# Performance work log

Measured on AMD Instinct MI355X. Metric: run time of the kernel, lower is better.

Reference implementation:

```python
import jax, jax.numpy as jnp
import numpy as np

B, S, E, H = 2, 2048, 1024, 16
D = E // H


def setup_inputs() -> dict:
    key = jax.random.key(0)
    ks = jax.random.split(key, 11)
    def lin(k):
        kw, kb = jax.random.split(k)
        bound = 1.0 / np.sqrt(E)
        W = jax.random.uniform(kw, (E, E), jnp.float32, -bound, bound)
        b = jax.random.uniform(kb, (E,), jnp.float32, -bound, bound)
        return W, b
    Wq, bq = lin(ks[0])
    Wk, bk = lin(ks[1])
    Wv, bv = lin(ks[2])
    Wo, bo = lin(ks[3])
    return {
        "query": jax.random.normal(ks[4], (B, S, E), jnp.float32),
        "key": jax.random.normal(ks[5], (B, S, E), jnp.float32),
        "value": jax.random.normal(ks[6], (B, S, E), jnp.float32),
        "Wq": Wq, "bq": bq, "Wk": Wk, "bk": bk,
        "Wv": Wv, "bv": bv, "Wo": Wo, "bo": bo,
        "is_causal": 1,
    }


def reference(query, key, value, Wq, bq, Wk, bk, Wv, bv, Wo, bo, is_causal):
    scale = D ** -0.5
    def heads(x, W, b):
        # torch Linear: x @ W.T + b, then [B,S,H,D] -> [B,H,S,D]
        y = jnp.einsum('bse,fe->bsf', x, W) + b
        return y.reshape(B, S, H, D).transpose(0, 2, 1, 3)
    q = heads(query, Wq, bq)
    k = heads(key, Wk, bk)
    v = heads(value, Wv, bv)
    scores = jnp.einsum('bhqd,bhkd->bhqk', q, k) * scale  # [B,H,S,S]
    if is_causal:
        mask = jnp.tril(jnp.ones((S, S), dtype=bool))
        scores = jnp.where(mask, scores, -jnp.inf)
    attn = jax.nn.softmax(scores, axis=-1)
    out = jnp.einsum('bhqk,bhkd->bhqd', attn, v)
    out = out.transpose(0, 2, 1, 3).reshape(B, S, E)
    return jnp.einsum('bse,fe->bsf', out, Wo) + bo
```

## Files before the change

kernel.cpp:

```cpp
#include <hip/hip_runtime.h>
#include <cstdint>
#include <cstddef>

typedef unsigned short u16;
typedef unsigned int u32;
typedef __attribute__((ext_vector_type(8))) short bf16x8;
typedef __attribute__((ext_vector_type(4))) float f32x4;
typedef __attribute__((ext_vector_type(16))) float f32x16;
typedef __attribute__((ext_vector_type(4))) u16 u16x4;
typedef __attribute__((ext_vector_type(4))) u32 u32x4;
typedef __attribute__((ext_vector_type(2))) u32 u32x2;

__device__ __forceinline__ u16 f2bf(float f) {
  u32 x = __builtin_bit_cast(u32, f);
  x += 0x7fffu + ((x >> 16) & 1u);
  return (u16)(x >> 16);
}

__device__ __forceinline__ void g2lds16(const u16* g, u16* l) {
  __builtin_amdgcn_global_load_lds(
      (const __attribute__((address_space(1))) u32*)g,
      (__attribute__((address_space(3))) u32*)l, 16, 0, 0);
}

struct CvtArgs { const float* s[7]; u16* d[7]; int n4[7]; };

__global__ __launch_bounds__(256) void cvt_all(CvtArgs a) {
  int y = blockIdx.y;
  const float4* __restrict__ src = (const float4*)a.s[y];
  u16* __restrict__ dst = a.d[y];
  int n4 = a.n4[y];
  for (int i = blockIdx.x * blockDim.x + threadIdx.x; i < n4;
       i += gridDim.x * blockDim.x) {
    float4 v = src[i];
    u16x4 o = { f2bf(v.x), f2bf(v.y), f2bf(v.z), f2bf(v.w) };
    *(u16x4*)(dst + (size_t)i * 4) = o;
  }
}

struct GemmArgs {
  const u16* A[3]; const u16* W[3]; const float* bias[3];
  void* out[3]; float scale[3]; int mode[3];
};

__global__ __launch_bounds__(256) void gemm_fused(GemmArgs ga) {
  __shared__ alignas(16) u16 As[2][128 * 32];
  __shared__ alignas(16) u16 Bs[2][128 * 32];
  const int z = blockIdx.z;
  const u16* __restrict__ A = ga.A[z];
  const u16* __restrict__ W = ga.W[z];
  const int tid = threadIdx.x;
  const int lane = tid & 63;
  const int w = tid >> 6;
  const int lo4 = lane & 15, hi2 = lane >> 4;
  const int l = (int)blockIdx.x + 8 * (int)blockIdx.y;
  const int wl = (l & 7) * 32 + (l >> 3);
  const int m0 = (wl >> 3) * 128;
  const int n0 = (wl & 7) * 128;
  const int wr = w >> 1, wc = w & 1;

  f32x4 acc[4][4] = {};

  auto stage = [&](int kt, int buf) {
    const int k0 = kt * 32;
#pragma unroll
    for (int i = 0; i < 2; ++i) {
      int c = (i * 4 + w) * 64 + lane;
      int r = c >> 2;
      int q = (c & 3) ^ ((r >> 1) & 3);
      g2lds16(A + (size_t)(m0 + r) * 1024 + k0 + q * 8, As[buf] + (i * 4 + w) * 512);
      g2lds16(W + (size_t)(n0 + r) * 1024 + k0 + q * 8, Bs[buf] + (i * 4 + w) * 512);
    }
  };

  stage(0, 0);
  stage(1, 1);
  for (int kt = 0; kt < 32; ++kt) {
    const int cur = kt & 1;
    asm volatile("s_waitcnt vmcnt(4)" ::: "memory");
    __builtin_amdgcn_s_barrier();
    bf16x8 af[4], bfr[4];
#pragma unroll
    for (int i = 0; i < 4; ++i) {
      int r = wr * 64 + i * 16 + lo4;
      int q = hi2 ^ ((r >> 1) & 3);
      af[i] = *(const bf16x8*)(As[cur] + r * 32 + q * 8);
    }
#pragma unroll
    for (int j = 0; j < 4; ++j) {
      int r = wc * 64 + j * 16 + lo4;
      int q = hi2 ^ ((r >> 1) & 3);
      bfr[j] = *(const bf16x8*)(Bs[cur] + r * 32 + q * 8);
    }
#pragma unroll
    for (int i = 0; i < 4; ++i)
#pragma unroll
      for (int j = 0; j < 4; ++j)
        acc[i][j] = __builtin_amdgcn_mfma_f32_16x16x32_bf16(af[i], bfr[j], acc[i][j], 0, 0, 0);
    __builtin_amdgcn_s_barrier();
    stage(kt + 2 < 32 ? kt + 2 : kt, cur);
  }
  asm volatile("s_waitcnt vmcnt(0)" ::: "memory");

  const float* __restrict__ bias = ga.bias[z];
  const float cs = ga.scale[z];
  const int mode = ga.mode[z];
#pragma unroll
  for (int j = 0; j < 4; ++j) {
    int n = n0 + wc * 64 + j * 16 + lo4;
    float bv = bias[n];
#pragma unroll
    for (int i = 0; i < 4; ++i) {
#pragma unroll
      for (int rg = 0; rg < 4; ++rg) {
        int m = m0 + wr * 64 + i * 16 + hi2 * 4 + rg;
        float v = (acc[i][j][rg] + bv) * cs;
        if (mode == 2) {
          ((float*)ga.out[z])[(size_t)m * 1024 + n] = v;
        } else {
          int b = m >> 11, s = m & 2047, h = n >> 6, d = n & 63;
          size_t addr = (mode == 0)
            ? ((size_t)(b * 16 + h) * 2048 + s) * 64 + d
            : ((size_t)(b * 16 + h) * 64 + d) * 2048 + s;
          ((u16*)ga.out[z])[addr] = f2bf(v);
        }
      }
    }
  }
}

__global__ __launch_bounds__(256, 2) void attn_kernel(
    const u16* __restrict__ Q, const u16* __restrict__ K,
    const u16* __restrict__ Vt, u16* __restrict__ Out,
    const int* __restrict__ causal_p) {
  __shared__ alignas(16) u16 Ks[2][2][64 * 64];
  __shared__ alignas(16) u16 Vs[2][2][64 * 64];
  const int tid = threadIdx.x, lane = tid & 63, w = tid >> 6;
  const int wg = w >> 1, wv = w & 1;
  const int ql = lane & 31, hi = lane >> 5;
  const int L = (int)blockIdx.x + 16 * (int)blockIdx.y;
  const int j = L >> 3;
  const int bh = (L & 7) * 4 + (j >> 4);
  const int slot = j & 15;
  const int qt = (j < 32) ? slot : 15 - slot;
  const int causal = *causal_p;
  const u16* Qb = Q + (size_t)bh * 2048 * 64;
  const u16* Kb = K + (size_t)bh * 2048 * 64;
  const u16* Vb = Vt + (size_t)bh * 64 * 2048;

  const int qA = qt * 128 + wv * 64 + ql;
  const int qB = qA + 32;

  bf16x8 qfA[4], qfB[4];
#pragma unroll
  for (int dsl = 0; dsl < 4; ++dsl) {
    qfA[dsl] = *(const bf16x8*)(Qb + (size_t)qA * 64 + dsl * 16 + hi * 8);
    qfB[dsl] = *(const bf16x8*)(Qb + (size_t)qB * 64 + dsl * 16 + hi * 8);
  }

  auto stageKV = [&](int jt, int buf) {
#pragma unroll
    for (int i = 0; i < 4; ++i) {
      int c = i * 128 + wv * 64 + lane;
      int r = c >> 3;
      int q = (c & 7) ^ (r & 7);
      g2lds16(Kb + (size_t)(jt * 64 + r) * 64 + q * 8, Ks[wg][buf] + (i * 128 + wv * 64) * 8);
      g2lds16(Vb + (size_t)r * 2048 + jt * 64 + q * 8, Vs[wg][buf] + (i * 128 + wv * 64) * 8);
    }
  };

  const int nt_w = causal ? (2 * qt + wv + 1) : 32;
  const int U = causal ? (qt + 1) : 16;

  stageKV(wg, 0);
  stageKV(wg + 2, 1);

  float mA = -1e30f, lA = 0.f, mB = -1e30f, lB = 0.f;
  f32x16 oA0 = {}, oA1 = {}, oB0 = {}, oB1 = {};

  auto online_sm = [&](f32x16& s0, f32x16& s1, float& m_r, float& l_r,
                       f32x16& o0, f32x16& o1) {
    float pm = fmaxf(s0[0], s1[0]);
#pragma unroll
    for (int rg = 1; rg < 16; ++rg) pm = fmaxf(pm, fmaxf(s0[rg], s1[rg]));
    pm = fmaxf(pm, __shfl_xor(pm, 32));
    if (!__all(pm <= m_r + 8.f)) {
      float mn = fmaxf(m_r, pm);
      float corr = exp2f(m_r - mn);
      m_r = mn; l_r *= corr;
#pragma unroll
      for (int rg = 0; rg < 16; ++rg) { o0[rg] *= corr; o1[rg] *= corr; }
    }
    float sum = 0.f;
#pragma unroll
    for (int rg = 0; rg < 16; ++rg) { s0[rg] = exp2f(s0[rg] - m_r); sum += s0[rg]; }
#pragma unroll
    for (int rg = 0; rg < 16; ++rg) { s1[rg] = exp2f(s1[rg] - m_r); sum += s1[rg]; }
    sum += __shfl_xor(sum, 32);
    l_r += sum;
  };

  for (int u = 0; u < U; ++u) {
    const int jt = 2 * u + wg;
    const int cur = u & 1;
    asm volatile("s_waitcnt vmcnt(8)" ::: "memory");
    __builtin_amdgcn_s_barrier();

    if (jt < nt_w) {
      f32x16 sA0 = {}, sA1 = {}, sB0 = {}, sB1 = {};
#pragma unroll
      for (int dsl = 0; dsl < 4; ++dsl) {
        int cc = dsl * 2 + hi;
        bf16x8 k0 = *(const bf16x8*)(Ks[wg][cur] + ql * 64 + ((cc ^ (ql & 7)) * 8));
        bf16x8 k1 = *(const bf16x8*)(Ks[wg][cur] + (32 + ql) * 64 + ((cc ^ (ql & 7)) * 8));
        sA0 = __builtin_amdgcn_mfma_f32_32x32x16_bf16(k0, qfA[dsl], sA0, 0, 0, 0);
        sB0 = __builtin_amdgcn_mfma_f32_32x32x16_bf16(k0, qfB[dsl], sB0, 0, 0, 0);
        sA1 = __builtin_amdgcn_mfma_f32_32x32x16_bf16(k1, qfA[dsl], sA1, 0, 0, 0);
        sB1 = __builtin_amdgcn_mfma_f32_32x32x16_bf16(k1, qfB[dsl], sB1, 0, 0, 0);
      }

      if (causal && jt == nt_w - 1) {
#pragma unroll
        for (int rg = 0; rg < 16; ++rg) {
          int kof = jt * 64 + 8 * (rg >> 2) + (rg & 3) + 4 * hi;
          sA0[rg] = (kof > qA) ? -1e30f : sA0[rg];
          sA1[rg] = (kof + 32 > qA) ? -1e30f : sA1[rg];
          sB0[rg] = (kof > qB) ? -1e30f : sB0[rg];
          sB1[rg] = (kof + 32 > qB) ? -1e30f : sB1[rg];
        }
      }

      online_sm(sA0, sA1, mA, lA, oA0, oA1);
      online_sm(sB0, sB1, mB, lB, oB0, oB1);

#pragma unroll
      for (int s = 0; s < 4; ++s) {
        const f32x16& pA = (s >= 2) ? sA1 : sA0;
        const f32x16& pB = (s >= 2) ? sB1 : sB0;
        const int base = 8 * (s & 1);
        u32 a0, a1, b0, b1, c0, c1, d0_, d1;
        asm("v_cvt_pk_bf16_f32 %0, %1, %2" : "=v"(a0) : "v"(pA[base + 0]), "v"(pA[base + 1]));
        asm("v_cvt_pk_bf16_f32 %0, %1, %2" : "=v"(a1) : "v"(pA[base + 2]), "v"(pA[base + 3]));
        asm("v_cvt_pk_bf16_f32 %0, %1, %2" : "=v"(b0) : "v"(pA[base + 4]), "v"(pA[base + 5]));
        asm("v_cvt_pk_bf16_f32 %0, %1, %2" : "=v"(b1) : "v"(pA[base + 6]), "v"(pA[base + 7]));
        asm volatile("v_permlane32_swap_b32 %0, %1" : "+v"(a0), "+v"(b0));
        asm volatile("v_permlane32_swap_b32 %0, %1" : "+v"(a1), "+v"(b1));
        asm("v_cvt_pk_bf16_f32 %0, %1, %2" : "=v"(c0) : "v"(pB[base + 0]), "v"(pB[base + 1]));
        asm("v_cvt_pk_bf16_f32 %0, %1, %2" : "=v"(c1) : "v"(pB[base + 2]), "v"(pB[base + 3]));
        asm("v_cvt_pk_bf16_f32 %0, %1, %2" : "=v"(d0_) : "v"(pB[base + 4]), "v"(pB[base + 5]));
        asm("v_cvt_pk_bf16_f32 %0, %1, %2" : "=v"(d1) : "v"(pB[base + 6]), "v"(pB[base + 7]));
        asm volatile("v_permlane32_swap_b32 %0, %1" : "+v"(c0), "+v"(d0_));
        asm volatile("v_permlane32_swap_b32 %0, %1" : "+v"(c1), "+v"(d1));
        u32x4 pwA = {a0, a1, b0, b1};
        u32x4 pwB = {c0, c1, d0_, d1};
        bf16x8 pfA = __builtin_bit_cast(bf16x8, pwA);
        bf16x8 pfB = __builtin_bit_cast(bf16x8, pwB);
#pragma unroll
        for (int df = 0; df < 2; ++df) {
          int rr = df * 32 + ql;
          bf16x8 vf = *(const bf16x8*)(Vs[wg][cur] + rr * 64 + (((s * 2 + hi) ^ (rr & 7)) * 8));
          if (df) {
            oA1 = __builtin_amdgcn_mfma_f32_32x32x16_bf16(vf, pfA, oA1, 0, 0, 0);
            oB1 = __builtin_amdgcn_mfma_f32_32x32x16_bf16(vf, pfB, oB1, 0, 0, 0);
          } else {
            oA0 = __builtin_amdgcn_mfma_f32_32x32x16_bf16(vf, pfA, oA0, 0, 0, 0);
            oB0 = __builtin_amdgcn_mfma_f32_32x32x16_bf16(vf, pfB, oB0, 0, 0, 0);
          }
        }
      }
    }
    __builtin_amdgcn_s_barrier();
    stageKV(u + 2 < U ? jt + 4 : jt, cur);
  }
  asm volatile("s_waitcnt vmcnt(0)" ::: "memory");
  __syncthreads();

  float* Od = (float*)&Ks[0][0][0];
  float* ml = (float*)&Vs[0][0][0];
  const int li = wv * 64 + lane;
  if (wg == 1) {
#pragma unroll
    for (int rg = 0; rg < 16; ++rg) {
      Od[((li * 2 + 0) * 2 + 0) * 16 + rg] = oA0[rg];
      Od[((li * 2 + 0) * 2 + 1) * 16 + rg] = oA1[rg];
      Od[((li * 2 + 1) * 2 + 0) * 16 + rg] = oB0[rg];
      Od[((li * 2 + 1) * 2 + 1) * 16 + rg] = oB1[rg];
    }
    ml[li * 4 + 0] = mA; ml[li * 4 + 1] = lA;
    ml[li * 4 + 2] = mB; ml[li * 4 + 3] = lB;
  }
  __syncthreads();
  if (wg == 0) {
    const int batch = bh >> 4, h = bh & 15;
#pragma unroll
    for (int sub = 0; sub < 2; ++sub) {
      float m_r = sub ? mB : mA;
      float l_r = sub ? lB : lA;
      float m_b = ml[li * 4 + sub * 2 + 0];
      float l_b = ml[li * 4 + sub * 2 + 1];
      float mn = fmaxf(m_r, m_b);
      float ca = exp2f(m_r - mn), cb = exp2f(m_b - mn);
      float rl = 1.f / (l_r * ca + l_b * cb);
      int qrow = sub ? qB : qA;
      u16* orow = Out + ((size_t)(batch * 2048 + qrow)) * 1024 + h * 64;
#pragma unroll
      for (int df = 0; df < 2; ++df) {
        const f32x16& oo = sub ? (df ? oB1 : oB0) : (df ? oA1 : oA0);
        const float* Op = &Od[((li * 2 + sub) * 2 + df) * 16];
#pragma unroll
        for (int b2 = 0; b2 < 4; ++b2) {
          u32 w0, w1;
          float v0 = (oo[4 * b2 + 0] * ca + Op[4 * b2 + 0] * cb) * rl;
          float v1 = (oo[4 * b2 + 1] * ca + Op[4 * b2 + 1] * cb) * rl;
          float v2 = (oo[4 * b2 + 2] * ca + Op[4 * b2 + 2] * cb) * rl;
          float v3 = (oo[4 * b2 + 3] * ca + Op[4 * b2 + 3] * cb) * rl;
          asm("v_cvt_pk_bf16_f32 %0, %1, %2" : "=v"(w0) : "v"(v0), "v"(v1));
          asm("v_cvt_pk_bf16_f32 %0, %1, %2" : "=v"(w1) : "v"(v2), "v"(v3));
          int d0 = df * 32 + b2 * 8 + hi * 4;
          u32x2 pr = {w0, w1};
          *(u32x2*)(orow + d0) = pr;
        }
      }
    }
  }
}

extern "C" void kernel_launch(void* const* d_in, const int* in_sizes, int n_in,
                              void* d_out, int out_size, void* d_ws, size_t ws_size,
                              hipStream_t stream) {
  (void)in_sizes; (void)n_in; (void)out_size; (void)ws_size;
  const float* query = (const float*)d_in[0];
  const float* key   = (const float*)d_in[1];
  const float* value = (const float*)d_in[2];
  const float* Wq = (const float*)d_in[3];
  const float* bq = (const float*)d_in[4];
  const float* Wk = (const float*)d_in[5];
  const float* bk = (const float*)d_in[6];
  const float* Wv = (const float*)d_in[7];
  const float* bv = (const float*)d_in[8];
  const float* Wo = (const float*)d_in[9];
  const float* bo = (const float*)d_in[10];
  const int* is_causal = (const int*)d_in[11];

  u16* wsp = (u16*)d_ws;
  u16* xq  = wsp;
  u16* xk  = xq  + (4u << 20);
  u16* xv  = xk  + (4u << 20);
  u16* wq  = xv  + (4u << 20);
  u16* wk  = wq  + (1u << 20);
  u16* wv  = wk  + (1u << 20);
  u16* wo  = wv  + (1u << 20);
  u16* Qb  = wo  + (1u << 20);
  u16* Kb  = Qb  + (4u << 20);
  u16* Vtb = Kb  + (4u << 20);
  u16* attn= Vtb + (4u << 20);

  CvtArgs ca;
  ca.s[0] = query; ca.d[0] = xq; ca.n4[0] = 1 << 20;
  ca.s[1] = key;   ca.d[1] = xk; ca.n4[1] = 1 << 20;
  ca.s[2] = value; ca.d[2] = xv; ca.n4[2] = 1 << 20;
  ca.s[3] = Wq; ca.d[3] = wq; ca.n4[3] = 1 << 18;
  ca.s[4] = Wk; ca.d[4] = wk; ca.n4[4] = 1 << 18;
  ca.s[5] = Wv; ca.d[5] = wv; ca.n4[5] = 1 << 18;
  ca.s[6] = Wo; ca.d[6] = wo; ca.n4[6] = 1 << 18;
  cvt_all<<<dim3(512, 7), 256, 0, stream>>>(ca);

  const float LOG2E = 1.4426950408889634f;
  GemmArgs g1;
  g1.A[0] = xq; g1.W[0] = wq; g1.bias[0] = bq; g1.out[0] = Qb;
  g1.scale[0] = 0.125f * LOG2E; g1.mode[0] = 0;
  g1.A[1] = xk; g1.W[1] = wk; g1.bias[1] = bk; g1.out[1] = Kb;
  g1.scale[1] = 1.f; g1.mode[1] = 0;
  g1.A[2] = xv; g1.W[2] = wv; g1.bias[2] = bv; g1.out[2] = Vtb;
  g1.scale[2] = 1.f; g1.mode[2] = 1;
  gemm_fused<<<dim3(8, 32, 3), 256, 0, stream>>>(g1);

  attn_kernel<<<dim3(16, 32), 256, 0, stream>>>(Qb, Kb, Vtb, attn, is_causal);

  GemmArgs g2;
  for (int i = 0; i < 3; ++i) {
    g2.A[i] = attn; g2.W[i] = wo; g2.bias[i] = bo; g2.out[i] = d_out;
    g2.scale[i] = 1.f; g2.mode[i] = 2;
  }
  gemm_fused<<<dim3(8, 32, 1), 256, 0, stream>>>(g2);
}
```

Before: 134.9 us.

## Split attention KV loop across four wave groups with 32-key tiles

The attention kernel moves from 256 to 512 threads, splitting the KV sequence across four wave groups that each handle 32-key tiles instead of two groups handling 64-key tiles. LDS staging, V layout swizzle, causal tile counts and masking are adjusted to match. The final combine merges the four partial softmax states sequentially through shared memory. This adds KV-level parallelism per block and halves per-wave register tiles, at the cost of more barriers, a longer merge epilogue and smaller MFMA work per iteration.

```diff
diff --git a/kernel.cpp b/kernel.cpp
--- a/kernel.cpp
+++ b/kernel.cpp
@@ -129,12 +129,12 @@
   }
 }
 
-__global__ __launch_bounds__(256, 2) void attn_kernel(
+__global__ __launch_bounds__(512, 4) void attn_kernel(
     const u16* __restrict__ Q, const u16* __restrict__ K,
     const u16* __restrict__ Vt, u16* __restrict__ Out,
     const int* __restrict__ causal_p) {
-  __shared__ alignas(16) u16 Ks[2][2][64 * 64];
-  __shared__ alignas(16) u16 Vs[2][2][64 * 64];
+  __shared__ alignas(16) u16 Ks[4][2][32 * 64];
+  __shared__ alignas(16) u16 Vs[4][2][64 * 32];
   const int tid = threadIdx.x, lane = tid & 63, w = tid >> 6;
   const int wg = w >> 1, wv = w & 1;
   const int ql = lane & 31, hi = lane >> 5;
@@ -160,29 +160,32 @@
 
   auto stageKV = [&](int jt, int buf) {
 #pragma unroll
-    for (int i = 0; i < 4; ++i) {
+    for (int i = 0; i < 2; ++i) {
       int c = i * 128 + wv * 64 + lane;
-      int r = c >> 3;
-      int q = (c & 7) ^ (r & 7);
-      g2lds16(Kb + (size_t)(jt * 64 + r) * 64 + q * 8, Ks[wg][buf] + (i * 128 + wv * 64) * 8);
-      g2lds16(Vb + (size_t)r * 2048 + jt * 64 + q * 8, Vs[wg][buf] + (i * 128 + wv * 64) * 8);
+      int r = c >> 3, s = c & 7;
+      int sl = s ^ (r & 7);
+      g2lds16(Kb + (size_t)(jt * 32 + r) * 64 + sl * 8,
+              Ks[wg][buf] + (i * 128 + wv * 64) * 8);
+      int d = 2 * r + (sl >> 2), c2 = sl & 3;
+      g2lds16(Vb + (size_t)d * 2048 + jt * 32 + c2 * 8,
+              Vs[wg][buf] + (i * 128 + wv * 64) * 8);
     }
   };
 
-  const int nt_w = causal ? (2 * qt + wv + 1) : 32;
-  const int U = causal ? (qt + 1) : 16;
+  const int nt_w = causal ? (4 * qt + 2 * wv + 2) : 32;
+  const int U = causal ? (qt + 1) : 8;
 
   stageKV(wg, 0);
-  stageKV(wg + 2, 1);
+  stageKV(wg + 4, 1);
 
   float mA = -1e30f, lA = 0.f, mB = -1e30f, lB = 0.f;
   f32x16 oA0 = {}, oA1 = {}, oB0 = {}, oB1 = {};
 
-  auto online_sm = [&](f32x16& s0, f32x16& s1, float& m_r, float& l_r,
+  auto online_sm = [&](f32x16& s0, float& m_r, float& l_r,
                        f32x16& o0, f32x16& o1) {
-    float pm = fmaxf(s0[0], s1[0]);
-#pragma unroll
-    for (int rg = 1; rg < 16; ++rg) pm = fmaxf(pm, fmaxf(s0[rg], s1[rg]));
+    float pm = s0[0];
+#pragma unroll
+    for (int rg = 1; rg < 16; ++rg) pm = fmaxf(pm, s0[rg]);
     pm = fmaxf(pm, __shfl_xor(pm, 32));
     if (!__all(pm <= m_r + 8.f)) {
       float mn = fmaxf(m_r, pm);
@@ -194,61 +197,52 @@
     float sum = 0.f;
 #pragma unroll
     for (int rg = 0; rg < 16; ++rg) { s0[rg] = exp2f(s0[rg] - m_r); sum += s0[rg]; }
-#pragma unroll
-    for (int rg = 0; rg < 16; ++rg) { s1[rg] = exp2f(s1[rg] - m_r); sum += s1[rg]; }
     sum += __shfl_xor(sum, 32);
     l_r += sum;
   };
 
   for (int u = 0; u < U; ++u) {
-    const int jt = 2 * u + wg;
+    const int jt = 4 * u + wg;
     const int cur = u & 1;
-    asm volatile("s_waitcnt vmcnt(8)" ::: "memory");
+    asm volatile("s_waitcnt vmcnt(4)" ::: "memory");
     __builtin_amdgcn_s_barrier();
 
     if (jt < nt_w) {
-      f32x16 sA0 = {}, sA1 = {}, sB0 = {}, sB1 = {};
+      f32x16 sA0 = {}, sB0 = {};
 #pragma unroll
       for (int dsl = 0; dsl < 4; ++dsl) {
         int cc = dsl * 2 + hi;
         bf16x8 k0 = *(const bf16x8*)(Ks[wg][cur] + ql * 64 + ((cc ^ (ql & 7)) * 8));
-        bf16x8 k1 = *(const bf16x8*)(Ks[wg][cur] + (32 + ql) * 64 + ((cc ^ (ql & 7)) * 8));
         sA0 = __builtin_amdgcn_mfma_f32_32x32x16_bf16(k0, qfA[dsl], sA0, 0, 0, 0);
         sB0 = __builtin_amdgcn_mfma_f32_32x32x16_bf16(k0, qfB[dsl], sB0, 0, 0, 0);
-        sA1 = __builtin_amdgcn_mfma_f32_32x32x16_bf16(k1, qfA[dsl], sA1, 0, 0, 0);
-        sB1 = __builtin_amdgcn_mfma_f32_32x32x16_bf16(k1, qfB[dsl], sB1, 0, 0, 0);
       }
 
-      if (causal && jt == nt_w - 1) {
+      if (causal && u == qt) {
 #pragma unroll
         for (int rg = 0; rg < 16; ++rg) {
-          int kof = jt * 64 + 8 * (rg >> 2) + (rg & 3) + 4 * hi;
+          int kof = jt * 32 + (rg & 3) + 8 * (rg >> 2) + 4 * hi;
           sA0[rg] = (kof > qA) ? -1e30f : sA0[rg];
-          sA1[rg] = (kof + 32 > qA) ? -1e30f : sA1[rg];
           sB0[rg] = (kof > qB) ? -1e30f : sB0[rg];
-          sB1[rg] = (kof + 32 > qB) ? -1e30f : sB1[rg];
         }
       }
 
-      online_sm(sA0, sA1, mA, lA, oA0, oA1);
-      online_sm(sB0, sB1, mB, lB, oB0, oB1);
-
-#pragma unroll
-      for (int s = 0; s < 4; ++s) {
-        const f32x16& pA = (s >= 2) ? sA1 : sA0;
-        const f32x16& pB = (s >= 2) ? sB1 : sB0;
-        const int base = 8 * (s & 1);
+      online_sm(sA0, mA, lA, oA0, oA1);
+      online_sm(sB0, mB, lB, oB0, oB1);
+
+#pragma unroll
+      for (int ks = 0; ks < 2; ++ks) {
+        const int base = 8 * ks;
         u32 a0, a1, b0, b1, c0, c1, d0_, d1;
-        asm("v_cvt_pk_bf16_f32 %0, %1, %2" : "=v"(a0) : "v"(pA[base + 0]), "v"(pA[base + 1]));
-        asm("v_cvt_pk_bf16_f32 %0, %1, %2" : "=v"(a1) : "v"(pA[base + 2]), "v"(pA[base + 3]));
-        asm("v_cvt_pk_bf16_f32 %0, %1, %2" : "=v"(b0) : "v"(pA[base + 4]), "v"(pA[base + 5]));
-        asm("v_cvt_pk_bf16_f32 %0, %1, %2" : "=v"(b1) : "v"(pA[base + 6]), "v"(pA[base + 7]));
+        asm("v_cvt_pk_bf16_f32 %0, %1, %2" : "=v"(a0) : "v"(sA0[base + 0]), "v"(sA0[base + 1]));
+        asm("v_cvt_pk_bf16_f32 %0, %1, %2" : "=v"(a1) : "v"(sA0[base + 2]), "v"(sA0[base + 3]));
+        asm("v_cvt_pk_bf16_f32 %0, %1, %2" : "=v"(b0) : "v"(sA0[base + 4]), "v"(sA0[base + 5]));
+        asm("v_cvt_pk_bf16_f32 %0, %1, %2" : "=v"(b1) : "v"(sA0[base + 6]), "v"(sA0[base + 7]));
         asm volatile("v_permlane32_swap_b32 %0, %1" : "+v"(a0), "+v"(b0));
         asm volatile("v_permlane32_swap_b32 %0, %1" : "+v"(a1), "+v"(b1));
-        asm("v_cvt_pk_bf16_f32 %0, %1, %2" : "=v"(c0) : "v"(pB[base + 0]), "v"(pB[base + 1]));
-        asm("v_cvt_pk_bf16_f32 %0, %1, %2" : "=v"(c1) : "v"(pB[base + 2]), "v"(pB[base + 3]));
-        asm("v_cvt_pk_bf16_f32 %0, %1, %2" : "=v"(d0_) : "v"(pB[base + 4]), "v"(pB[base + 5]));
-        asm("v_cvt_pk_bf16_f32 %0, %1, %2" : "=v"(d1) : "v"(pB[base + 6]), "v"(pB[base + 7]));
+        asm("v_cvt_pk_bf16_f32 %0, %1, %2" : "=v"(c0) : "v"(sB0[base + 0]), "v"(sB0[base + 1]));
+        asm("v_cvt_pk_bf16_f32 %0, %1, %2" : "=v"(c1) : "v"(sB0[base + 2]), "v"(sB0[base + 3]));
+        asm("v_cvt_pk_bf16_f32 %0, %1, %2" : "=v"(d0_) : "v"(sB0[base + 4]), "v"(sB0[base + 5]));
+        asm("v_cvt_pk_bf16_f32 %0, %1, %2" : "=v"(d1) : "v"(sB0[base + 6]), "v"(sB0[base + 7]));
         asm volatile("v_permlane32_swap_b32 %0, %1" : "+v"(c0), "+v"(d0_));
         asm volatile("v_permlane32_swap_b32 %0, %1" : "+v"(c1), "+v"(d1));
         u32x4 pwA = {a0, a1, b0, b1};
@@ -258,7 +252,9 @@
 #pragma unroll
         for (int df = 0; df < 2; ++df) {
           int rr = df * 32 + ql;
-          bf16x8 vf = *(const bf16x8*)(Vs[wg][cur] + rr * 64 + (((s * 2 + hi) ^ (rr & 7)) * 8));
+          int sl = (rr & 1) * 4 + ks * 2 + hi;
+          const bf16x8 vf = *(const bf16x8*)(
+              Vs[wg][cur] + ((rr >> 1) * 8 + (sl ^ ((rr >> 1) & 7))) * 8);
           if (df) {
             oA1 = __builtin_amdgcn_mfma_f32_32x32x16_bf16(vf, pfA, oA1, 0, 0, 0);
             oB1 = __builtin_amdgcn_mfma_f32_32x32x16_bf16(vf, pfB, oB1, 0, 0, 0);
@@ -270,50 +266,74 @@
       }
     }
     __builtin_amdgcn_s_barrier();
-    stageKV(u + 2 < U ? jt + 4 : jt, cur);
+    stageKV(u + 2 < U ? jt + 8 : jt, cur);
   }
   asm volatile("s_waitcnt vmcnt(0)" ::: "memory");
   __syncthreads();
 
   float* Od = (float*)&Ks[0][0][0];
-  float* ml = (float*)&Vs[0][0][0];
+  float* ml = Od + 8192;
   const int li = wv * 64 + lane;
-  if (wg == 1) {
+
+  auto store_partial = [&]() {
 #pragma unroll
     for (int rg = 0; rg < 16; ++rg) {
-      Od[((li * 2 + 0) * 2 + 0) * 16 + rg] = oA0[rg];
-      Od[((li * 2 + 0) * 2 + 1) * 16 + rg] = oA1[rg];
-      Od[((li * 2 + 1) * 2 + 0) * 16 + rg] = oB0[rg];
-      Od[((li * 2 + 1) * 2 + 1) * 16 + rg] = oB1[rg];
+      Od[li * 64 + rg]      = oA0[rg];
+      Od[li * 64 + 16 + rg] = oA1[rg];
+      Od[li * 64 + 32 + rg] = oB0[rg];
+      Od[li * 64 + 48 + rg] = oB1[rg];
     }
     ml[li * 4 + 0] = mA; ml[li * 4 + 1] = lA;
     ml[li * 4 + 2] = mB; ml[li * 4 + 3] = lB;
-  }
-  __syncthreads();
+  };
+  auto merge_partial = [&]() {
+    float m_b = ml[li * 4 + 0], l_b = ml[li * 4 + 1];
+    float mn = fmaxf(mA, m_b);
+    float ca = exp2f(mA - mn), cb = exp2f(m_b - mn);
+    mA = mn; lA = lA * ca + l_b * cb;
+#pragma unroll
+    for (int rg = 0; rg < 16; ++rg) {
+      oA0[rg] = oA0[rg] * ca + Od[li * 64 + rg] * cb;
+      oA1[rg] = oA1[rg] * ca + Od[li * 64 + 16 + rg] * cb;
+    }
+    m_b = ml[li * 4 + 2]; l_b = ml[li * 4 + 3];
+    mn = fmaxf(mB, m_b);
+    ca = exp2f(mB - mn); cb = exp2f(m_b - mn);
+    mB = mn; lB = lB * ca + l_b * cb;
+#pragma unroll
+    for (int rg = 0; rg < 16; ++rg) {
+      oB0[rg] = oB0[rg] * ca + Od[li * 64 + 32 + rg] * cb;
+      oB1[rg] = oB1[rg] * ca + Od[li * 64 + 48 + rg] * cb;
+    }
+  };
+
+  if (wg == 1) store_partial();
+  __syncthreads();
+  if (wg == 0) merge_partial();
+  __syncthreads();
+  if (wg == 2) store_partial();
+  __syncthreads();
+  if (wg == 0) merge_partial();
+  __syncthreads();
+  if (wg == 3) store_partial();
+  __syncthreads();
+
   if (wg == 0) {
+    merge_partial();
     const int batch = bh >> 4, h = bh & 15;
 #pragma unroll
     for (int sub = 0; sub < 2; ++sub) {
-      float m_r = sub ? mB : mA;
-      float l_r = sub ? lB : lA;
-      float m_b = ml[li * 4 + sub * 2 + 0];
-      float l_b = ml[li * 4 + sub * 2 + 1];
-      float mn = fmaxf(m_r, m_b);
-      float ca = exp2f(m_r - mn), cb = exp2f(m_b - mn);
-      float rl = 1.f / (l_r * ca + l_b * cb);
+      float rl = 1.f / (sub ? lB : lA);
       int qrow = sub ? qB : qA;
       u16* orow = Out + ((size_t)(batch * 2048 + qrow)) * 1024 + h * 64;
 #pragma unroll
       for (int df = 0; df < 2; ++df) {
         const f32x16& oo = sub ? (df ? oB1 : oB0) : (df ? oA1 : oA0);
-        const float* Op = &Od[((li * 2 + sub) * 2 + df) * 16];
 #pragma unroll
         for (int b2 = 0; b2 < 4; ++b2) {
           u32 w0, w1;
-          float v0 = (oo[4 * b2 + 0] * ca + Op[4 * b2 + 0] * cb) * rl;
-          float v1 = (oo[4 * b2 + 1] * ca + Op[4 * b2 + 1] * cb) * rl;
-          float v2 = (oo[4 * b2 + 2] * ca + Op[4 * b2 + 2] * cb) * rl;
-          float v3 = (oo[4 * b2 + 3] * ca + Op[4 * b2 + 3] * cb) * rl;
+          float v0 = oo[4 * b2 + 0] * rl, v1 = oo[4 * b2 + 1] * rl;
+          float v2 = oo[4 * b2 + 2] * rl, v3 = oo[4 * b2 + 3] * rl;
           asm("v_cvt_pk_bf16_f32 %0, %1, %2" : "=v"(w0) : "v"(v0), "v"(v1));
           asm("v_cvt_pk_bf16_f32 %0, %1, %2" : "=v"(w1) : "v"(v2), "v"(v3));
           int d0 = df * 32 + b2 * 8 + hi * 4;
@@ -375,7 +395,7 @@
   g1.scale[2] = 1.f; g1.mode[2] = 1;
   gemm_fused<<<dim3(8, 32, 3), 256, 0, stream>>>(g1);
 
-  attn_kernel<<<dim3(16, 32), 256, 0, stream>>>(Qb, Kb, Vtb, attn, is_causal);
+  attn_kernel<<<dim3(16, 32), 512, 0, stream>>>(Qb, Kb, Vtb, attn, is_causal);
 
   GemmArgs g2;
   for (int i = 0; i < 3; ++i) {
```

Result: slower. 187.7 us (+39.1%).

## Load V fragments directly from global into registers, halve LDS for occupancy

Applied to the files above, without the earlier changes.

Removes the LDS staging buffer for V tiles and instead has each wave load its V fragments straight from global memory into registers at the start of each tile iteration. The freed LDS (and a small separate buffer for m/l) lets launch bounds rise from 2 to 3 blocks per CU. The vmcnt wait is adjusted to match fewer in-flight async loads. The cost is unhidden global-load latency for V inside the loop, since V is no longer prefetched ahead, plus more register pressure under a tighter register budget.

```diff
diff --git a/kernel.cpp b/kernel.cpp
--- a/kernel.cpp
+++ b/kernel.cpp
@@ -129,12 +129,12 @@
   }
 }
 
-__global__ __launch_bounds__(256, 2) void attn_kernel(
+__global__ __launch_bounds__(256, 3) void attn_kernel(
     const u16* __restrict__ Q, const u16* __restrict__ K,
     const u16* __restrict__ Vt, u16* __restrict__ Out,
     const int* __restrict__ causal_p) {
   __shared__ alignas(16) u16 Ks[2][2][64 * 64];
-  __shared__ alignas(16) u16 Vs[2][2][64 * 64];
+  __shared__ float ml2[512];
   const int tid = threadIdx.x, lane = tid & 63, w = tid >> 6;
   const int wg = w >> 1, wv = w & 1;
   const int ql = lane & 31, hi = lane >> 5;
@@ -158,22 +158,21 @@
     qfB[dsl] = *(const bf16x8*)(Qb + (size_t)qB * 64 + dsl * 16 + hi * 8);
   }
 
-  auto stageKV = [&](int jt, int buf) {
+  auto stageK = [&](int jt, int buf) {
 #pragma unroll
     for (int i = 0; i < 4; ++i) {
       int c = i * 128 + wv * 64 + lane;
       int r = c >> 3;
       int q = (c & 7) ^ (r & 7);
       g2lds16(Kb + (size_t)(jt * 64 + r) * 64 + q * 8, Ks[wg][buf] + (i * 128 + wv * 64) * 8);
-      g2lds16(Vb + (size_t)r * 2048 + jt * 64 + q * 8, Vs[wg][buf] + (i * 128 + wv * 64) * 8);
     }
   };
 
   const int nt_w = causal ? (2 * qt + wv + 1) : 32;
   const int U = causal ? (qt + 1) : 16;
 
-  stageKV(wg, 0);
-  stageKV(wg + 2, 1);
+  stageK(wg, 0);
+  stageK(wg + 2, 1);
 
   float mA = -1e30f, lA = 0.f, mB = -1e30f, lB = 0.f;
   f32x16 oA0 = {}, oA1 = {}, oB0 = {}, oB1 = {};
@@ -203,10 +202,17 @@
   for (int u = 0; u < U; ++u) {
     const int jt = 2 * u + wg;
     const int cur = u & 1;
-    asm volatile("s_waitcnt vmcnt(8)" ::: "memory");
+    asm volatile("s_waitcnt vmcnt(4)" ::: "memory");
     __builtin_amdgcn_s_barrier();
 
     if (jt < nt_w) {
+      bf16x8 vr0[4], vr1[4];
+#pragma unroll
+      for (int s = 0; s < 4; ++s) {
+        vr0[s] = *(const bf16x8*)(Vb + (size_t)ql * 2048 + jt * 64 + (s * 2 + hi) * 8);
+        vr1[s] = *(const bf16x8*)(Vb + (size_t)(32 + ql) * 2048 + jt * 64 + (s * 2 + hi) * 8);
+      }
+
       f32x16 sA0 = {}, sA1 = {}, sB0 = {}, sB1 = {};
 #pragma unroll
       for (int dsl = 0; dsl < 4; ++dsl) {
@@ -255,28 +261,20 @@
         u32x4 pwB = {c0, c1, d0_, d1};
         bf16x8 pfA = __builtin_bit_cast(bf16x8, pwA);
         bf16x8 pfB = __builtin_bit_cast(bf16x8, pwB);
-#pragma unroll
-        for (int df = 0; df < 2; ++df) {
-          int rr = df * 32 + ql;
-          bf16x8 vf = *(const bf16x8*)(Vs[wg][cur] + rr * 64 + (((s * 2 + hi) ^ (rr & 7)) * 8));
-          if (df) {
-            oA1 = __builtin_amdgcn_mfma_f32_32x32x16_bf16(vf, pfA, oA1, 0, 0, 0);
-            oB1 = __builtin_amdgcn_mfma_f32_32x32x16_bf16(vf, pfB, oB1, 0, 0, 0);
-          } else {
-            oA0 = __builtin_amdgcn_mfma_f32_32x32x16_bf16(vf, pfA, oA0, 0, 0, 0);
-            oB0 = __builtin_amdgcn_mfma_f32_32x32x16_bf16(vf, pfB, oB0, 0, 0, 0);
-          }
-        }
+        oA0 = __builtin_amdgcn_mfma_f32_32x32x16_bf16(vr0[s], pfA, oA0, 0, 0, 0);
+        oB0 = __builtin_amdgcn_mfma_f32_32x32x16_bf16(vr0[s], pfB, oB0, 0, 0, 0);
+        oA1 = __builtin_amdgcn_mfma_f32_32x32x16_bf16(vr1[s], pfA, oA1, 0, 0, 0);
+        oB1 = __builtin_amdgcn_mfma_f32_32x32x16_bf16(vr1[s], pfB, oB1, 0, 0, 0);
       }
     }
     __builtin_amdgcn_s_barrier();
-    stageKV(u + 2 < U ? jt + 4 : jt, cur);
+    stageK(u + 2 < U ? jt + 4 : jt, cur);
   }
   asm volatile("s_waitcnt vmcnt(0)" ::: "memory");
   __syncthreads();
 
   float* Od = (float*)&Ks[0][0][0];
-  float* ml = (float*)&Vs[0][0][0];
+  float* ml = ml2;
   const int li = wv * 64 + lane;
   if (wg == 1) {
 #pragma unroll
```

Measured after the change: 228.0 us. 1.69x slower.
